# Kernel optimization log

Measured on AMD Instinct MI355X. Metric: run time of the kernel, lower is better.

The kernel has to match this reference:

```python
import jax, jax.numpy as jnp
import numpy as np

N_SAMPLES = 128
AGENTS = 64
D = 128          # latent_size
EDIM = 2         # edge attr dim
N = N_SAMPLES * AGENTS
EPS = 1e-5


def _build_edges():
    a = np.arange(AGENTS)
    rows = np.repeat(a, AGENTS)
    cols = np.tile(a, AGENTS)
    mask = rows != cols  # fully connected, no self loops
    rows, cols = rows[mask], cols[mask]
    offsets = (np.arange(N_SAMPLES) * AGENTS)[:, None]
    src = (rows[None, :] + offsets).ravel().astype(np.int32)  # edge_index[0]
    dst = (cols[None, :] + offsets).ravel().astype(np.int32)  # edge_index[1]
    return src, dst


def setup_inputs() -> dict:
    key = jax.random.key(0)
    ks = jax.random.split(key, 16)
    src, dst = _build_edges()
    zin = 2 * D + EDIM  # CGConv concat [x_i, x_j, e]
    inp = {
        "gnn_in": jax.random.normal(ks[0], (N, D), jnp.float32),
        "centers": jax.random.normal(ks[1], (N, EDIM), jnp.float32),
        "edge_src": jnp.asarray(src),
        "edge_dst": jnp.asarray(dst),
    }
    for li, base in ((1, 2), (2, 8)):
        inp[f"Wf{li}"] = jax.random.normal(ks[base + 0], (zin, D), jnp.float32) / np.sqrt(zin)
        inp[f"bf{li}"] = jnp.zeros((D,), jnp.float32)
        inp[f"Ws{li}"] = jax.random.normal(ks[base + 1], (zin, D), jnp.float32) / np.sqrt(zin)
        inp[f"bs{li}"] = jnp.zeros((D,), jnp.float32)
        inp[f"gamma{li}"] = jnp.ones((D,), jnp.float32)
        inp[f"beta{li}"] = jnp.zeros((D,), jnp.float32)
    return inp


def _cgconv(x, e, src, dst, Wf, bf, Ws, bs, gamma, beta):
    # message: z = [x_i(target), x_j(source), e]; sigmoid(Wf z) * softplus(Ws z)
    z = jnp.concatenate([x[dst], x[src], e], axis=-1)  # [E, 2D+2]
    m = jax.nn.sigmoid(z @ Wf + bf) * jax.nn.softplus(z @ Ws + bs)
    agg = jax.ops.segment_sum(m, dst, num_segments=N)  # scatter-add at targets
    # batch norm (training-mode batch stats) then residual, as in PyG CGConv
    mu = agg.mean(axis=0)
    var = agg.var(axis=0)
    agg = (agg - mu) * jax.lax.rsqrt(var + EPS) * gamma + beta
    return agg + x


def reference(gnn_in, centers, edge_src, edge_dst,
              Wf1, bf1, Ws1, bs1, gamma1, beta1,
              Wf2, bf2, Ws2, bs2, gamma2, beta2):
    # edge_attr = centers[col] - centers[row]
    e = centers[edge_dst] - centers[edge_src]  # [E, 2]
    x = jax.nn.relu(_cgconv(gnn_in, e, edge_src, edge_dst, Wf1, bf1, Ws1, bs1, gamma1, beta1))
    x = jax.nn.relu(_cgconv(x, e, edge_src, edge_dst, Wf2, bf2, Ws2, bs2, gamma2, beta2))
    return x
```

## Files before the change

kernel.cpp:

```cpp
#include <hip/hip_runtime.h>
#include <hip/hip_bf16.h>

#define NSAMP 128
#define AGENTS 64
#define D 128
#define NN (NSAMP * AGENTS)
#define LOG2E 1.44269504088896340736f
#define LN2   0.69314718055994530942f
#define EPSF  1e-5f

typedef __attribute__((ext_vector_type(8))) short short8;
typedef __attribute__((ext_vector_type(4))) float floatx4;

__device__ __forceinline__ float u2f(unsigned v) {
    float f; __builtin_memcpy(&f, &v, 4); return f;
}
__device__ __forceinline__ unsigned f2u(float f) {
    unsigned v; __builtin_memcpy(&v, &f, 4); return v;
}
__device__ __forceinline__ unsigned short f2bf(float f) {
    unsigned x; __builtin_memcpy(&x, &f, 4);
    return (unsigned short)((x + 0x7FFFu + ((x >> 16) & 1u)) >> 16);
}

__global__ __launch_bounds__(256) void cvt_kernel(
    const float* __restrict__ Wf1, const float* __restrict__ Ws1,
    const float* __restrict__ Wf2, const float* __restrict__ Ws2,
    unsigned short* __restrict__ WT, float* __restrict__ sacc)
{
    int t = blockIdx.x, tid = threadIdx.x;
    if (t < 64) {
        int rr = t * 16 + (tid >> 4);
        int kk = (tid & 15) * 8;
        int layer = rr >> 9, rem = rr & 511, arr = rem >> 7, c = rem & 127;
        const float* M = (arr < 2) ? (layer ? Wf2 : Wf1) : (layer ? Ws2 : Ws1);
        int side = arr & 1;
        short8 sv;
        #pragma unroll
        for (int j = 0; j < 8; ++j)
            sv[j] = (short)f2bf(M[(size_t)(side * 128 + kk + j) * D + c]);
        *(short8*)&WT[(size_t)(layer * 4 + arr) * 16384 + c * 128 + kk] = sv;
    } else {
        sacc[tid]       = 0.f;
        sacc[256 + tid] = 0.f;
    }
}

__global__ __launch_bounds__(512, 8) void prep_edge(
    const float* __restrict__ xin,
    const unsigned short* __restrict__ WTl,
    const float* __restrict__ centers,
    const float* __restrict__ Wf, const float* __restrict__ bfp,
    const float* __restrict__ Ws, const float* __restrict__ bsp,
    float* __restrict__ agg,
    float* __restrict__ sa)
{
    const int s = blockIdx.x >> 3, q = blockIdx.x & 7;
    const int nbase = s * AGENTS;
    const int tid = threadIdx.x;
    const int w = tid >> 6, lane = tid & 63;
    const int quad = lane >> 4, l16 = lane & 15;
    const int m = w & 3, pair = w >> 2;
    const int col = q * 16 + l16;

    __shared__ unsigned int EApk[64][17];
    __shared__ unsigned int EBpk[64][17];

    short8 a[4];
    {
        const float* xr = xin + (size_t)(nbase + m * 16 + l16) * D + quad * 8;
        #pragma unroll
        for (int kc = 0; kc < 4; ++kc) {
            float4 v0 = *(const float4*)(xr + kc * 32);
            float4 v1 = *(const float4*)(xr + kc * 32 + 4);
            short8 tv;
            tv[0] = (short)f2bf(v0.x); tv[1] = (short)f2bf(v0.y);
            tv[2] = (short)f2bf(v0.z); tv[3] = (short)f2bf(v0.w);
            tv[4] = (short)f2bf(v1.x); tv[5] = (short)f2bf(v1.y);
            tv[6] = (short)f2bf(v1.z); tv[7] = (short)f2bf(v1.w);
            a[kc] = tv;
        }
    }
    const int arrF = pair ? 0 : 1, arrS = pair ? 2 : 3;
    floatx4 accF = {0.f,0.f,0.f,0.f}, accS = {0.f,0.f,0.f,0.f};
    {
        const unsigned short* wpF = WTl + ((size_t)arrF * 128 + col) * 128 + quad * 8;
        const unsigned short* wpS = WTl + ((size_t)arrS * 128 + col) * 128 + quad * 8;
        #pragma unroll
        for (int kc = 0; kc < 4; ++kc) {
            accF = __builtin_amdgcn_mfma_f32_16x16x32_bf16(
                a[kc], *(const short8*)(wpF + kc * 32), accF, 0, 0, 0);
            accS = __builtin_amdgcn_mfma_f32_16x16x32_bf16(
                a[kc], *(const short8*)(wpS + kc * 32), accS, 0, 0, 0);
        }
    }
    {
        const float cwf0 = Wf[256 * D + col], cwf1 = Wf[257 * D + col];
        const float cws0 = Ws[256 * D + col], cws1 = Ws[257 * D + col];
        const float bfv = bfp[col], bsv = bsp[col];
        #pragma unroll
        for (int r = 0; r < 4; ++r) {
            int row = m * 16 + quad * 4 + r;
            int n = nbase + row;
            float ce0 = centers[2 * n], ce1 = centers[2 * n + 1];
            float ctf = fmaf(ce0, cwf0, ce1 * cwf1);
            float cts = fmaf(ce0, cws0, ce1 * cws1);
            if (pair) {
                unsigned uf = (unsigned)f2bf(__builtin_amdgcn_exp2f(-LOG2E * (accF[r] + ctf + bfv)));
                unsigned us = (unsigned)f2bf(__builtin_amdgcn_exp2f( LOG2E * (accS[r] + cts + bsv)));
                EApk[row][l16] = uf | (us << 16);
            } else {
                unsigned uf = (unsigned)f2bf(__builtin_amdgcn_exp2f(-LOG2E * (accF[r] - ctf)));
                unsigned us = (unsigned)f2bf(__builtin_amdgcn_exp2f( LOG2E * (accS[r] - cts)));
                EBpk[row][l16] = uf | (us << 16);
            }
        }
    }
    __syncthreads();

    const int cl = tid & 15, slot = tid >> 4;
    const int c = q * 16 + cl;
    float eaf[2], eas[2], ac2[2];
    #pragma unroll
    for (int i = 0; i < 2; ++i) {
        unsigned pk = EApk[slot * 2 + i][cl];
        eaf[i] = u2f(pk << 16);
        eas[i] = u2f(pk & 0xFFFF0000u);
        ac2[i] = 0.f;
    }
    #pragma unroll 8
    for (int j = 0; j < 64; ++j) {
        unsigned pk = EBpk[j][cl];
        float ebf = u2f(pk << 16);
        float ebs = u2f(pk & 0xFFFF0000u);
        #pragma unroll
        for (int i = 0; i < 2; ++i) {
            float sg = __builtin_amdgcn_rcpf(fmaf(eaf[i], ebf, 1.f));
            float lg = __builtin_amdgcn_logf(fmaf(eas[i], ebs, 1.f));
            ac2[i] = fmaf(sg, lg, ac2[i]);
        }
    }
    float s1 = 0.f, s2 = 0.f;
    #pragma unroll
    for (int i = 0; i < 2; ++i) {
        int d = slot * 2 + i;
        unsigned pk = EBpk[d][cl];
        float ebf = u2f(pk << 16);
        float ebs = u2f(pk & 0xFFFF0000u);
        float sg = __builtin_amdgcn_rcpf(fmaf(eaf[i], ebf, 1.f));
        float lg = __builtin_amdgcn_logf(fmaf(eas[i], ebs, 1.f));
        float v = (ac2[i] - sg * lg) * LN2;
        agg[(size_t)(nbase + d) * D + c] = v;
        s1 += v; s2 += v * v;
    }
    __syncthreads();
    EApk[slot][cl] = f2u(s1);
    EBpk[slot][cl] = f2u(s2);
    __syncthreads();
    #pragma unroll
    for (int off = 16; off >= 1; off >>= 1) {
        if (slot < off) {
            EApk[slot][cl] = f2u(u2f(EApk[slot][cl]) + u2f(EApk[slot + off][cl]));
            EBpk[slot][cl] = f2u(u2f(EBpk[slot][cl]) + u2f(EBpk[slot + off][cl]));
        }
        __syncthreads();
    }
    if (slot == 0) {
        atomicAdd(&sa[c],       u2f(EApk[0][cl]));
        atomicAdd(&sa[128 + c], u2f(EBpk[0][cl]));
    }
}

__global__ __launch_bounds__(256) void bn_kernel(
    const float* __restrict__ agg, const float* __restrict__ xin,
    const float* __restrict__ sa,
    const float* __restrict__ gm, const float* __restrict__ bt,
    float* __restrict__ outp)
{
    const int idx = blockIdx.x * 256 + threadIdx.x;
    const int n = idx >> 4;
    const int c = (idx & 15) * 8;
    size_t off = (size_t)n * D + c;
    const float inv = 1.f / NN;
    float v[8];
    #pragma unroll
    for (int h = 0; h < 2; ++h) {
        float4 av  = *(const float4*)&agg[off + h * 4];
        float4 xv  = *(const float4*)&xin[off + h * 4];
        float4 s1v = *(const float4*)&sa[c + h * 4];
        float4 s2v = *(const float4*)&sa[128 + c + h * 4];
        float4 gmv = *(const float4*)&gm[c + h * 4];
        float4 btv = *(const float4*)&bt[c + h * 4];
        float mu, var, rs;
        mu = s1v.x * inv; var = s2v.x * inv - mu * mu; rs = rsqrtf(var + EPSF);
        v[h*4+0] = fmaxf(0.f, fmaf((av.x - mu) * rs, gmv.x, btv.x) + xv.x);
        mu = s1v.y * inv; var = s2v.y * inv - mu * mu; rs = rsqrtf(var + EPSF);
        v[h*4+1] = fmaxf(0.f, fmaf((av.y - mu) * rs, gmv.y, btv.y) + xv.y);
        mu = s1v.z * inv; var = s2v.z * inv - mu * mu; rs = rsqrtf(var + EPSF);
        v[h*4+2] = fmaxf(0.f, fmaf((av.z - mu) * rs, gmv.z, btv.z) + xv.z);
        mu = s1v.w * inv; var = s2v.w * inv - mu * mu; rs = rsqrtf(var + EPSF);
        v[h*4+3] = fmaxf(0.f, fmaf((av.w - mu) * rs, gmv.w, btv.w) + xv.w);
    }
    *(float4*)&outp[off]     = *(float4*)&v[0];
    *(float4*)&outp[off + 4] = *(float4*)&v[4];
}

extern "C" void kernel_launch(void* const* d_in, const int* in_sizes, int n_in,
                              void* d_out, int out_size, void* d_ws, size_t ws_size,
                              hipStream_t stream) {
    const float* x0      = (const float*)d_in[0];
    const float* centers = (const float*)d_in[1];
    const float* Wf1 = (const float*)d_in[4];
    const float* bf1 = (const float*)d_in[5];
    const float* Ws1 = (const float*)d_in[6];
    const float* bs1 = (const float*)d_in[7];
    const float* gm1 = (const float*)d_in[8];
    const float* bt1 = (const float*)d_in[9];
    const float* Wf2 = (const float*)d_in[10];
    const float* bf2 = (const float*)d_in[11];
    const float* Ws2 = (const float*)d_in[12];
    const float* bs2 = (const float*)d_in[13];
    const float* gm2 = (const float*)d_in[14];
    const float* bt2 = (const float*)d_in[15];

    const size_t ND = (size_t)NN * D;
    unsigned short* ws_u = (unsigned short*)d_ws;
    unsigned short* WT = ws_u;
    float* fbase = (float*)(WT + 2 * 65536);
    float* agg   = fbase;
    float* x1    = fbase + ND;
    float* sacc  = fbase + 2 * ND;

    float* outp = (float*)d_out;

    cvt_kernel<<<dim3(65), dim3(256), 0, stream>>>(
        Wf1, Ws1, Wf2, Ws2, WT, sacc);

    prep_edge<<<dim3(1024), dim3(512), 0, stream>>>(
        x0, WT, centers, Wf1, bf1, Ws1, bs1, agg, sacc);
    bn_kernel<<<dim3(512), dim3(256), 0, stream>>>(
        agg, x0, sacc, gm1, bt1, x1);

    prep_edge<<<dim3(1024), dim3(512), 0, stream>>>(
        x1, WT + 65536, centers, Wf2, bf2, Ws2, bs2, agg, sacc + 256);
    bn_kernel<<<dim3(512), dim3(256), 0, stream>>>(
        agg, x1, sacc + 256, gm2, bt2, outp);
}
```

Baseline: 154.7 us.

## Process two samples per block with 4-row register tiles in edge kernel

Each block now handles two samples for one 16-column slice. Every wave computes all four projection arrays for its 16 rows, so one x fragment feeds four MFMA chains. Shared memory is transposed to [col][row] so the pairwise loop reads packed uint4 vectors, and each thread accumulates 4 target rows instead of 2, which cuts LDS loads per transcendental pair. The grid is halved and the occupancy hint drops from 8 to 4 blocks, trading parallelism and register pressure for fewer LDS loads and less per-block overhead.

```diff
diff --git a/kernel.cpp b/kernel.cpp
--- a/kernel.cpp
+++ b/kernel.cpp
@@ -14,9 +14,6 @@
 
 __device__ __forceinline__ float u2f(unsigned v) {
     float f; __builtin_memcpy(&f, &v, 4); return f;
-}
-__device__ __forceinline__ unsigned f2u(float f) {
-    unsigned v; __builtin_memcpy(&v, &f, 4); return v;
 }
 __device__ __forceinline__ unsigned short f2bf(float f) {
     unsigned x; __builtin_memcpy(&x, &f, 4);
@@ -46,7 +43,7 @@
     }
 }
 
-__global__ __launch_bounds__(512, 8) void prep_edge(
+__global__ __launch_bounds__(512, 4) void prep_edge(
     const float* __restrict__ xin,
     const unsigned short* __restrict__ WTl,
     const float* __restrict__ centers,
@@ -55,46 +52,44 @@
     float* __restrict__ agg,
     float* __restrict__ sa)
 {
-    const int s = blockIdx.x >> 3, q = blockIdx.x & 7;
-    const int nbase = s * AGENTS;
+    const int s0 = (blockIdx.x >> 3) * 2, q = blockIdx.x & 7;
     const int tid = threadIdx.x;
     const int w = tid >> 6, lane = tid & 63;
     const int quad = lane >> 4, l16 = lane & 15;
-    const int m = w & 3, pair = w >> 2;
     const int col = q * 16 + l16;
 
-    __shared__ unsigned int EApk[64][17];
-    __shared__ unsigned int EBpk[64][17];
-
-    short8 a[4];
+    __shared__ unsigned int EApk[2][16][68];
+    __shared__ unsigned int EBpk[2][16][68];
+
     {
-        const float* xr = xin + (size_t)(nbase + m * 16 + l16) * D + quad * 8;
-        #pragma unroll
-        for (int kc = 0; kc < 4; ++kc) {
-            float4 v0 = *(const float4*)(xr + kc * 32);
-            float4 v1 = *(const float4*)(xr + kc * 32 + 4);
-            short8 tv;
-            tv[0] = (short)f2bf(v0.x); tv[1] = (short)f2bf(v0.y);
-            tv[2] = (short)f2bf(v0.z); tv[3] = (short)f2bf(v0.w);
-            tv[4] = (short)f2bf(v1.x); tv[5] = (short)f2bf(v1.y);
-            tv[6] = (short)f2bf(v1.z); tv[7] = (short)f2bf(v1.w);
-            a[kc] = tv;
-        }
-    }
-    const int arrF = pair ? 0 : 1, arrS = pair ? 2 : 3;
-    floatx4 accF = {0.f,0.f,0.f,0.f}, accS = {0.f,0.f,0.f,0.f};
-    {
-        const unsigned short* wpF = WTl + ((size_t)arrF * 128 + col) * 128 + quad * 8;
-        const unsigned short* wpS = WTl + ((size_t)arrS * 128 + col) * 128 + quad * 8;
-        #pragma unroll
-        for (int kc = 0; kc < 4; ++kc) {
-            accF = __builtin_amdgcn_mfma_f32_16x16x32_bf16(
-                a[kc], *(const short8*)(wpF + kc * 32), accF, 0, 0, 0);
-            accS = __builtin_amdgcn_mfma_f32_16x16x32_bf16(
-                a[kc], *(const short8*)(wpS + kc * 32), accS, 0, 0, 0);
-        }
-    }
-    {
+        const int smp = w >> 2, m = w & 3;
+        const int nbase = (s0 + smp) * AGENTS;
+        short8 a[4];
+        {
+            const float* xr = xin + (size_t)(nbase + m * 16 + l16) * D + quad * 8;
+            #pragma unroll
+            for (int kc = 0; kc < 4; ++kc) {
+                float4 v0 = *(const float4*)(xr + kc * 32);
+                float4 v1 = *(const float4*)(xr + kc * 32 + 4);
+                short8 tv;
+                tv[0] = (short)f2bf(v0.x); tv[1] = (short)f2bf(v0.y);
+                tv[2] = (short)f2bf(v0.z); tv[3] = (short)f2bf(v0.w);
+                tv[4] = (short)f2bf(v1.x); tv[5] = (short)f2bf(v1.y);
+                tv[6] = (short)f2bf(v1.z); tv[7] = (short)f2bf(v1.w);
+                a[kc] = tv;
+            }
+        }
+        floatx4 acc[4];
+        #pragma unroll
+        for (int arr = 0; arr < 4; ++arr) {
+            const unsigned short* wp = WTl + ((size_t)arr * 128 + col) * 128 + quad * 8;
+            floatx4 ac = {0.f, 0.f, 0.f, 0.f};
+            #pragma unroll
+            for (int kc = 0; kc < 4; ++kc)
+                ac = __builtin_amdgcn_mfma_f32_16x16x32_bf16(
+                    a[kc], *(const short8*)(wp + kc * 32), ac, 0, 0, 0);
+            acc[arr] = ac;
+        }
         const float cwf0 = Wf[256 * D + col], cwf1 = Wf[257 * D + col];
         const float cws0 = Ws[256 * D + col], cws1 = Ws[257 * D + col];
         const float bfv = bfp[col], bsv = bsp[col];
@@ -105,69 +100,81 @@
             float ce0 = centers[2 * n], ce1 = centers[2 * n + 1];
             float ctf = fmaf(ce0, cwf0, ce1 * cwf1);
             float cts = fmaf(ce0, cws0, ce1 * cws1);
-            if (pair) {
-                unsigned uf = (unsigned)f2bf(__builtin_amdgcn_exp2f(-LOG2E * (accF[r] + ctf + bfv)));
-                unsigned us = (unsigned)f2bf(__builtin_amdgcn_exp2f( LOG2E * (accS[r] + cts + bsv)));
-                EApk[row][l16] = uf | (us << 16);
-            } else {
-                unsigned uf = (unsigned)f2bf(__builtin_amdgcn_exp2f(-LOG2E * (accF[r] - ctf)));
-                unsigned us = (unsigned)f2bf(__builtin_amdgcn_exp2f( LOG2E * (accS[r] - cts)));
-                EBpk[row][l16] = uf | (us << 16);
+            unsigned eafu = (unsigned)f2bf(__builtin_amdgcn_exp2f(-LOG2E * (acc[0][r] + ctf + bfv)));
+            unsigned easu = (unsigned)f2bf(__builtin_amdgcn_exp2f( LOG2E * (acc[2][r] + cts + bsv)));
+            unsigned ebfu = (unsigned)f2bf(__builtin_amdgcn_exp2f(-LOG2E * (acc[1][r] - ctf)));
+            unsigned ebsu = (unsigned)f2bf(__builtin_amdgcn_exp2f( LOG2E * (acc[3][r] - cts)));
+            EApk[smp][l16][row] = eafu | (easu << 16);
+            EBpk[smp][l16][row] = ebfu | (ebsu << 16);
+        }
+    }
+    __syncthreads();
+
+    const int cl = tid & 15, slot = tid >> 4;
+    const int smpB = slot >> 4;
+    const int r0 = (slot & 15) * 4;
+    const int nb2 = (s0 + smpB) * AGENTS;
+    const int c = q * 16 + cl;
+
+    float eaf[4], eas[4], ac2[4];
+    {
+        uint4 ea4 = *(const uint4*)&EApk[smpB][cl][r0];
+        unsigned ew[4] = {ea4.x, ea4.y, ea4.z, ea4.w};
+        #pragma unroll
+        for (int i = 0; i < 4; ++i) {
+            eaf[i] = u2f(ew[i] << 16);
+            eas[i] = u2f(ew[i] & 0xFFFF0000u);
+            ac2[i] = 0.f;
+        }
+    }
+    #pragma unroll 2
+    for (int jb = 0; jb < 16; ++jb) {
+        uint4 pk4 = *(const uint4*)&EBpk[smpB][cl][jb * 4];
+        unsigned pkw[4] = {pk4.x, pk4.y, pk4.z, pk4.w};
+        #pragma unroll
+        for (int jj = 0; jj < 4; ++jj) {
+            float ebf = u2f(pkw[jj] << 16);
+            float ebs = u2f(pkw[jj] & 0xFFFF0000u);
+            #pragma unroll
+            for (int i = 0; i < 4; ++i) {
+                float sg = __builtin_amdgcn_rcpf(fmaf(eaf[i], ebf, 1.f));
+                float lg = __builtin_amdgcn_logf(fmaf(eas[i], ebs, 1.f));
+                ac2[i] = fmaf(sg, lg, ac2[i]);
             }
         }
     }
-    __syncthreads();
-
-    const int cl = tid & 15, slot = tid >> 4;
-    const int c = q * 16 + cl;
-    float eaf[2], eas[2], ac2[2];
-    #pragma unroll
-    for (int i = 0; i < 2; ++i) {
-        unsigned pk = EApk[slot * 2 + i][cl];
-        eaf[i] = u2f(pk << 16);
-        eas[i] = u2f(pk & 0xFFFF0000u);
-        ac2[i] = 0.f;
-    }
-    #pragma unroll 8
-    for (int j = 0; j < 64; ++j) {
-        unsigned pk = EBpk[j][cl];
-        float ebf = u2f(pk << 16);
-        float ebs = u2f(pk & 0xFFFF0000u);
-        #pragma unroll
-        for (int i = 0; i < 2; ++i) {
+    float s1 = 0.f, s2 = 0.f;
+    {
+        uint4 sd4 = *(const uint4*)&EBpk[smpB][cl][r0];
+        unsigned sw[4] = {sd4.x, sd4.y, sd4.z, sd4.w};
+        #pragma unroll
+        for (int i = 0; i < 4; ++i) {
+            float ebf = u2f(sw[i] << 16);
+            float ebs = u2f(sw[i] & 0xFFFF0000u);
             float sg = __builtin_amdgcn_rcpf(fmaf(eaf[i], ebf, 1.f));
             float lg = __builtin_amdgcn_logf(fmaf(eas[i], ebs, 1.f));
-            ac2[i] = fmaf(sg, lg, ac2[i]);
-        }
-    }
-    float s1 = 0.f, s2 = 0.f;
-    #pragma unroll
-    for (int i = 0; i < 2; ++i) {
-        int d = slot * 2 + i;
-        unsigned pk = EBpk[d][cl];
-        float ebf = u2f(pk << 16);
-        float ebs = u2f(pk & 0xFFFF0000u);
-        float sg = __builtin_amdgcn_rcpf(fmaf(eaf[i], ebf, 1.f));
-        float lg = __builtin_amdgcn_logf(fmaf(eas[i], ebs, 1.f));
-        float v = (ac2[i] - sg * lg) * LN2;
-        agg[(size_t)(nbase + d) * D + c] = v;
-        s1 += v; s2 += v * v;
+            float v = (ac2[i] - sg * lg) * LN2;
+            agg[(size_t)(nb2 + r0 + i) * D + c] = v;
+            s1 += v; s2 += v * v;
+        }
     }
     __syncthreads();
-    EApk[slot][cl] = f2u(s1);
-    EBpk[slot][cl] = f2u(s2);
+    float* red1 = (float*)&EApk[0][0][0];
+    float* red2 = (float*)&EBpk[0][0][0];
+    red1[slot * 16 + cl] = s1;
+    red2[slot * 16 + cl] = s2;
     __syncthreads();
     #pragma unroll
     for (int off = 16; off >= 1; off >>= 1) {
         if (slot < off) {
-            EApk[slot][cl] = f2u(u2f(EApk[slot][cl]) + u2f(EApk[slot + off][cl]));
-            EBpk[slot][cl] = f2u(u2f(EBpk[slot][cl]) + u2f(EBpk[slot + off][cl]));
+            red1[slot * 16 + cl] += red1[(slot + off) * 16 + cl];
+            red2[slot * 16 + cl] += red2[(slot + off) * 16 + cl];
         }
         __syncthreads();
     }
     if (slot == 0) {
-        atomicAdd(&sa[c],       u2f(EApk[0][cl]));
-        atomicAdd(&sa[128 + c], u2f(EBpk[0][cl]));
+        atomicAdd(&sa[c],       red1[cl]);
+        atomicAdd(&sa[128 + c], red2[cl]);
     }
 }
 
@@ -236,12 +243,12 @@
     cvt_kernel<<<dim3(65), dim3(256), 0, stream>>>(
         Wf1, Ws1, Wf2, Ws2, WT, sacc);
 
-    prep_edge<<<dim3(1024), dim3(512), 0, stream>>>(
+    prep_edge<<<dim3(512), dim3(512), 0, stream>>>(
         x0, WT, centers, Wf1, bf1, Ws1, bs1, agg, sacc);
     bn_kernel<<<dim3(512), dim3(256), 0, stream>>>(
         agg, x0, sacc, gm1, bt1, x1);
 
-    prep_edge<<<dim3(1024), dim3(512), 0, stream>>>(
+    prep_edge<<<dim3(512), dim3(512), 0, stream>>>(
         x1, WT + 65536, centers, Wf2, bf2, Ws2, bs2, agg, sacc + 256);
     bn_kernel<<<dim3(512), dim3(256), 0, stream>>>(
         agg, x1, sacc + 256, gm2, bt2, outp);
```

After: 149.5 us. -3.3%, faster.
